# Kernel optimization log

Hardware: AMD Instinct MI355X
Metric: run time of the kernel (lower is better)

The kernel has to match this reference:

```python
import jax, jax.numpy as jnp
import numpy as np
from jax import lax

B, T, IN, H = 128, 1024, 130, 512


def setup_inputs() -> dict:
    key = jax.random.key(0)
    ks = jax.random.split(key, 6)
    inputs = jax.random.normal(ks[0], (B, T, IN), dtype=jnp.float32)
    # valid lengths in [1, T] (forward indexes outputs[len-1])
    inputs_len = jax.random.randint(ks[1], (B,), 1, T + 1)
    h0 = jnp.zeros((B, H), dtype=jnp.float32)
    c0 = jnp.zeros((B, H), dtype=jnp.float32)
    s = 1.0 / np.sqrt(H)
    W_ih = jax.random.uniform(ks[2], (4 * H, IN - 2), jnp.float32, -s, s)
    W_hh = jax.random.uniform(ks[3], (4 * H, H), jnp.float32, -s, s)
    b_ih = jax.random.uniform(ks[4], (4 * H,), jnp.float32, -s, s)
    b_hh = jax.random.uniform(ks[5], (4 * H,), jnp.float32, -s, s)
    return {"inputs": inputs, "inputs_len": inputs_len, "h0": h0, "c0": c0,
            "W_ih": W_ih, "W_hh": W_hh, "b_ih": b_ih, "b_hh": b_hh}


def _lstm_encode(inputs, h0, c0, W_ih, W_hh, b_ih, b_hh):
    # drop last 2 features (coordinates), as in stard_LSTM branch
    x = inputs[..., :-2]                                   # [B, T, IN-2]
    # precompute input projections for all timesteps (same math as per-step)
    xproj = jnp.einsum('bti,gi->tbg', x, W_ih) + b_ih + b_hh  # [T, B, 4H]

    def step(carry, xw):
        h, c = carry
        gates = xw + h @ W_hh.T                            # [B, 4H]
        i, f, g, o = jnp.split(gates, 4, axis=-1)
        i = jax.nn.sigmoid(i)
        f = jax.nn.sigmoid(f)
        g = jnp.tanh(g)
        o = jax.nn.sigmoid(o)
        c2 = f * c + i * g
        h2 = o * jnp.tanh(c2)
        return (h2, c2), h2

    _, hs = lax.scan(step, (h0, c0), xproj)                # hs: [T, B, H]
    return hs


def reference(inputs, inputs_len, h0, c0, W_ih, W_hh, b_ih, b_hh):
    hs = _lstm_encode(inputs, h0, c0, W_ih, W_hh, b_ih, b_hh)
    # gather hidden state at last valid timestep per sequence
    b_idx = jnp.arange(inputs.shape[0])
    return hs[inputs_len - 1, b_idx]                       # [B, H]
```

## Files before the change

### kernel.cpp

```cpp
#include <hip/hip_runtime.h>
#include <hip/hip_bf16.h>
#include <cstdint>
#include <cstddef>

#define T_STEPS 1024
#define BATCH   128
#define INF     128
#define HID     512
#define NBLK    256
#define NTHR    256
#define PK      648

typedef _Float16 f16x8 __attribute__((ext_vector_type(8)));
typedef float    f32x4 __attribute__((ext_vector_type(4)));

static __device__ __forceinline__ unsigned short f16b(float v) {
  _Float16 h = (_Float16)v;
  unsigned short u;
  __builtin_memcpy(&u, &h, 2);
  return u;
}
static __device__ __forceinline__ float fsigmoid(float x) {
  return 1.f / (1.f + __expf(-x));
}
static __device__ __forceinline__ float ftanh(float x) {
  return 1.f - 2.f / (__expf(2.f * x) + 1.f);
}


__global__ __launch_bounds__(256) void k_prep_x(const float* __restrict__ in,
                                                unsigned short* __restrict__ xp)
{
  int t = blockIdx.x >> 3, bg = blockIdx.x & 7;
  int tid = threadIdx.x;
  size_t base = (size_t)blockIdx.x * 2048;
  #pragma unroll
  for (int rep = 0; rep < 8; ++rep) {
    int idx = rep * 256 + tid;
    int c = idx >> 7, k = idx & 127;
    float v = in[((size_t)(bg * 16 + c) * T_STEPS + t) * 130 + k];
    xp[base + c * 128 + k] = f16b(v);
  }
}

__global__ __launch_bounds__(64) void k_prep_w(const float* __restrict__ Wih,
                                               const float* __restrict__ Whh,
                                               unsigned short* __restrict__ wf)
{
  int blk = blockIdx.x;
  int s = blk % 20; int r = blk / 20;
  int u4 = r & 3; int ug = r >> 2;
  int l = threadIdx.x;
  int m = l & 15;
  int Grow = (m & 3) * HID + ug * 16 + u4 * 4 + (m >> 2);
  int kb = s * 32 + (l >> 4) * 8;
  unsigned short o[8];
  #pragma unroll
  for (int j = 0; j < 8; ++j) {
    float v = (kb + j < INF) ? Wih[(size_t)Grow * INF + kb + j]
                             : Whh[(size_t)Grow * HID + (kb + j - INF)];
    o[j] = f16b(v);
  }
  unsigned short* d = wf + ((size_t)blk * 64 + l) * 8;
  #pragma unroll
  for (int j = 0; j < 8; ++j) d[j] = o[j];
}

__global__ __launch_bounds__(256) void k_prep_h(const float* __restrict__ h0,
                                                unsigned long long* __restrict__ hp0,
                                                unsigned long long* __restrict__ hp1)
{
  int idx = blockIdx.x * 256 + threadIdx.x;
  int bg = idx >> 12;
  int r = idx & 4095;
  int c = r >> 8, u2 = r & 255;
  float v0 = h0[(size_t)(bg * 16 + c) * HID + 2 * u2];
  float v1 = h0[(size_t)(bg * 16 + c) * HID + 2 * u2 + 1];
  hp0[idx] = (unsigned long long)((unsigned)f16b(v0) | ((unsigned)f16b(v1) << 16));
  hp1[idx] = 0ull;
}

__global__ __launch_bounds__(NTHR, 1) void k_persist(
    const unsigned short* __restrict__ xp,
    const unsigned short* __restrict__ wf,
    const float* __restrict__ bih, const float* __restrict__ bhh,
    unsigned long long* __restrict__ hp0,
    unsigned long long* __restrict__ hp1,
    const float* __restrict__ c0,
    const int* __restrict__ len,
    float* __restrict__ out)
{
  __shared__ short zpl[2][16][PK];

  const int blk = blockIdx.x;
  const int ug = blk & 31, bg = blk >> 5;
  const int tid = threadIdx.x;
  const int w = tid >> 6, l = tid & 63;
  const int cB = l & 15, gch = l >> 4;

  const uint4* wfq = (const uint4*)wf;
  const int fb = (ug * 4 + w) * 20;
#define LDW(s_) (*reinterpret_cast<const f16x8*>(&wfq[(size_t)(fb + (s_)) * 64 + l]))
  f16x8 A0 = LDW(0),  A1 = LDW(1),  A2 = LDW(2),  A3 = LDW(3),  A4 = LDW(4);
  f16x8 A5 = LDW(5),  A6 = LDW(6),  A7 = LDW(7),  A8 = LDW(8),  A9 = LDW(9);
  f16x8 A10 = LDW(10), A11 = LDW(11), A12 = LDW(12), A13 = LDW(13), A14 = LDW(14);
  f16x8 A15 = LDW(15), A16 = LDW(16), A17 = LDW(17), A18 = LDW(18), A19 = LDW(19);
#undef LDW
  asm volatile("" : "+v"(A0), "+v"(A1), "+v"(A2), "+v"(A3), "+v"(A4),
                    "+v"(A5), "+v"(A6), "+v"(A7), "+v"(A8), "+v"(A9),
                    "+v"(A10), "+v"(A11), "+v"(A12), "+v"(A13), "+v"(A14),
                    "+v"(A15), "+v"(A16), "+v"(A17), "+v"(A18), "+v"(A19));

  const int cb = l & 15;
  const int uloc = l >> 4;
  const int hu = ug * 16 + w * 4 + uloc;
  const int gb = bg * 16 + cb;
  float c_reg = c0[(size_t)gb * HID + hu];
  const int mylen = len[gb];
  float bsq[4];
  #pragma unroll
  for (int g = 0; g < 4; ++g) bsq[g] = bih[g * HID + hu] + bhh[g * HID + hu];

  const int hc = tid >> 4, hs = tid & 15;

  for (int t = 0; t < T_STEPS; ++t) {
    const unsigned long long* hq = ((t & 1) ? hp1 : hp0) + (size_t)bg * 4096;
    unsigned long long*       hd = ((t & 1) ? hp0 : hp1) + (size_t)bg * 4096;
    short (*zb)[PK] = zpl[t & 1];

    uint4 xv = ((const uint4*)(xp + (size_t)(t * 8 + bg) * 2048))[tid];

    unsigned long long hch[16];
    #pragma unroll
    for (int j = 0; j < 16; ++j)
      hch[j] = __hip_atomic_load(hq + hc * 256 + j * 16 + hs,
                                 __ATOMIC_RELAXED, __HIP_MEMORY_SCOPE_AGENT);

    *(uint4*)((char*)&zb[tid >> 4][0] + (tid & 15) * 16) = xv;

    for (;;) {
      int bad = 0;
      #pragma unroll
      for (int j = 0; j < 16; ++j)
        if ((unsigned)(hch[j] >> 32) != (unsigned)t) bad = 1;
      if (!__any(bad)) break;
      __builtin_amdgcn_s_sleep(1);
      #pragma unroll
      for (int j = 0; j < 16; ++j)
        if ((unsigned)(hch[j] >> 32) != (unsigned)t)
          hch[j] = __hip_atomic_load(hq + hc * 256 + j * 16 + hs,
                                     __ATOMIC_RELAXED, __HIP_MEMORY_SCOPE_AGENT);
    }

    {
      unsigned* zr = (unsigned*)&zb[hc][128];
      #pragma unroll
      for (int j = 0; j < 16; ++j)
        zr[j * 16 + hs] = (unsigned)hch[j];
    }
    __syncthreads();

    f32x4 aE = {0, 0, 0, 0}, aO = {0, 0, 0, 0};
    const short* zr = &zb[cB][0];
#define KS(s_, AF, ACC) \
  { f16x8 B = *(const f16x8*)(zr + (s_) * 32 + gch * 8); \
    ACC = __builtin_amdgcn_mfma_f32_16x16x32_f16(AF, B, ACC, 0, 0, 0); }
    KS(0, A0, aE)  KS(1, A1, aO)  KS(2, A2, aE)  KS(3, A3, aO)
    KS(4, A4, aE)  KS(5, A5, aO)  KS(6, A6, aE)  KS(7, A7, aO)
    KS(8, A8, aE)  KS(9, A9, aO)  KS(10, A10, aE) KS(11, A11, aO)
    KS(12, A12, aE) KS(13, A13, aO) KS(14, A14, aE) KS(15, A15, aO)
    KS(16, A16, aE) KS(17, A17, aO) KS(18, A18, aE) KS(19, A19, aO)
#undef KS

    float s0 = aE[0] + aO[0] + bsq[0];
    float s1 = aE[1] + aO[1] + bsq[1];
    float s2 = aE[2] + aO[2] + bsq[2];
    float s3 = aE[3] + aO[3] + bsq[3];
    float iv = fsigmoid(s0);
    float fv = fsigmoid(s1);
    float gv = ftanh(s2);
    float ov = fsigmoid(s3);
    c_reg = fv * c_reg + iv * gv;
    float h2 = ov * ftanh(c_reg);

    unsigned hb = f16b(h2);
    unsigned other = __shfl_xor(hb, 16);
    if ((uloc & 1) == 0) {
      unsigned long long word = ((unsigned long long)(unsigned)(t + 1) << 32)
                              | (unsigned long long)(hb | (other << 16));
      __hip_atomic_store(hd + cb * 256 + (ug * 8 + w * 2 + (uloc >> 1)), word,
                         __ATOMIC_RELAXED, __HIP_MEMORY_SCOPE_AGENT);
    }
    if (t == mylen - 1) out[(size_t)gb * HID + hu] = h2;
  }
}

extern "C" void kernel_launch(void* const* d_in, const int* in_sizes, int n_in,
                              void* d_out, int out_size, void* d_ws, size_t ws_size,
                              hipStream_t stream)
{
  const float* inputs = (const float*)d_in[0];
  const int*   len    = (const int*)  d_in[1];
  const float* h0     = (const float*)d_in[2];
  const float* c0     = (const float*)d_in[3];
  const float* Wih    = (const float*)d_in[4];
  const float* Whh    = (const float*)d_in[5];
  const float* bih    = (const float*)d_in[6];
  const float* bhh    = (const float*)d_in[7];
  float* out = (float*)d_out;

  char* p = (char*)d_ws;
  unsigned short* xp = (unsigned short*)p; p += (size_t)T_STEPS * 8 * 2048 * 2;
  unsigned short* wf = (unsigned short*)p; p += (size_t)2560 * 64 * 8 * 2;
  unsigned long long* hp0 = (unsigned long long*)p; p += (size_t)8 * 4096 * 8;
  unsigned long long* hp1 = (unsigned long long*)p; p += (size_t)8 * 4096 * 8;

  k_prep_x<<<T_STEPS * 8, 256, 0, stream>>>(inputs, xp);
  k_prep_w<<<2560, 64, 0, stream>>>(Wih, Whh, wf);
  k_prep_h<<<128, 256, 0, stream>>>(h0, hp0, hp1);

  void* args[] = {(void*)&xp, (void*)&wf, (void*)&bih, (void*)&bhh,
                  (void*)&hp0, (void*)&hp1, (void*)&c0, (void*)&len,
                  (void*)&out};
  (void)hipLaunchCooperativeKernel((void*)k_persist, dim3(NBLK), dim3(NTHR),
                                   args, 0, stream);
}
```

Before: 3.452 ms.

## Interleave two batch groups per block to overlap h polling with compute

Each persistent block now handles two batch groups (A and B) with one set of register-resident weights, and the grid is halved to 128 blocks. The loop alternates between groups: while one group's MFMA and gate math run, the block issues and polls the other group's hidden-state loads, so cross-block synchronization latency is hidden behind useful work. In exchange, each block does twice the compute serially per step, with fewer blocks spread over the CUs.

```diff
diff --git a/kernel.cpp b/kernel.cpp
--- a/kernel.cpp
+++ b/kernel.cpp
@@ -7,7 +7,7 @@
 #define BATCH   128
 #define INF     128
 #define HID     512
-#define NBLK    256
+#define NBLK    128
 #define NTHR    256
 #define PK      648
 
@@ -90,10 +90,12 @@
     const int* __restrict__ len,
     float* __restrict__ out)
 {
-  __shared__ short zpl[2][16][PK];
+  __shared__ short zplA[16][PK];
+  __shared__ short zplB[16][PK];
 
   const int blk = blockIdx.x;
-  const int ug = blk & 31, bg = blk >> 5;
+  const int ug = blk & 31, pr = blk >> 5;
+  const int bgA = pr * 2, bgB = pr * 2 + 1;
   const int tid = threadIdx.x;
   const int w = tid >> 6, l = tid & 63;
   const int cB = l & 15, gch = l >> 4;
@@ -114,85 +116,129 @@
   const int cb = l & 15;
   const int uloc = l >> 4;
   const int hu = ug * 16 + w * 4 + uloc;
-  const int gb = bg * 16 + cb;
-  float c_reg = c0[(size_t)gb * HID + hu];
-  const int mylen = len[gb];
+  const int gbA = bgA * 16 + cb, gbB = bgB * 16 + cb;
+  float cA  = c0[(size_t)gbA * HID + hu];
+  float cB_ = c0[(size_t)gbB * HID + hu];
+  const int lenA = len[gbA], lenB = len[gbB];
   float bsq[4];
   #pragma unroll
   for (int g = 0; g < 4; ++g) bsq[g] = bih[g * HID + hu] + bhh[g * HID + hu];
 
   const int hc = tid >> 4, hs = tid & 15;
 
+#define HISSUE(HQ, HCH)                                                        \
+  _Pragma("unroll")                                                            \
+  for (int j = 0; j < 16; ++j)                                                 \
+    (HCH)[j] = __hip_atomic_load((HQ) + hc * 256 + j * 16 + hs,                \
+                                 __ATOMIC_RELAXED, __HIP_MEMORY_SCOPE_AGENT);
+
+#define HCHECK(HQ, HCH, TT)                                                    \
+  for (;;) {                                                                   \
+    int bad = 0;                                                               \
+    _Pragma("unroll")                                                          \
+    for (int j = 0; j < 16; ++j)                                               \
+      if ((unsigned)((HCH)[j] >> 32) != (unsigned)(TT)) bad = 1;               \
+    if (!__any(bad)) break;                                                    \
+    __builtin_amdgcn_s_sleep(1);                                               \
+    _Pragma("unroll")                                                          \
+    for (int j = 0; j < 16; ++j)                                               \
+      if ((unsigned)((HCH)[j] >> 32) != (unsigned)(TT))                        \
+        (HCH)[j] = __hip_atomic_load((HQ) + hc * 256 + j * 16 + hs,            \
+                                     __ATOMIC_RELAXED, __HIP_MEMORY_SCOPE_AGENT); \
+  }
+
+#define HSTAGE(ZB, HCH, XV)                                                    \
+  *(uint4*)((char*)&(ZB)[tid >> 4][0] + (tid & 15) * 16) = (XV);               \
+  {                                                                            \
+    unsigned* zr_ = (unsigned*)&(ZB)[hc][128];                                 \
+    _Pragma("unroll")                                                          \
+    for (int j = 0; j < 16; ++j) zr_[j * 16 + hs] = (unsigned)(HCH)[j];        \
+  }
+
+#define KS(ZR, s_, AF, ACC)                                                    \
+  { f16x8 B = *(const f16x8*)((ZR) + (s_) * 32 + gch * 8);                     \
+    ACC = __builtin_amdgcn_mfma_f32_16x16x32_f16(AF, B, ACC, 0, 0, 0); }
+
+#define COMPUTE(ZB, CREG, HD, GB, MYLEN)                                       \
+  {                                                                            \
+    f32x4 aE = {0, 0, 0, 0}, aO = {0, 0, 0, 0};                                \
+    const short* zr_ = &(ZB)[cB][0];                                           \
+    KS(zr_, 0, A0, aE)  KS(zr_, 1, A1, aO)  KS(zr_, 2, A2, aE)                 \
+    KS(zr_, 3, A3, aO)  KS(zr_, 4, A4, aE)  KS(zr_, 5, A5, aO)                 \
+    KS(zr_, 6, A6, aE)  KS(zr_, 7, A7, aO)  KS(zr_, 8, A8, aE)                 \
+    KS(zr_, 9, A9, aO)  KS(zr_, 10, A10, aE) KS(zr_, 11, A11, aO)              \
+    KS(zr_, 12, A12, aE) KS(zr_, 13, A13, aO) KS(zr_, 14, A14, aE)             \
+    KS(zr_, 15, A15, aO) KS(zr_, 16, A16, aE) KS(zr_, 17, A17, aO)             \
+    KS(zr_, 18, A18, aE) KS(zr_, 19, A19, aO)                                  \
+    float s0 = aE[0] + aO[0] + bsq[0];                                         \
+    float s1 = aE[1] + aO[1] + bsq[1];                                         \
+    float s2 = aE[2] + aO[2] + bsq[2];                                         \
+    float s3 = aE[3] + aO[3] + bsq[3];                                         \
+    float iv = fsigmoid(s0), fv = fsigmoid(s1);                                \
+    float gv = ftanh(s2),    ov = fsigmoid(s3);                                \
+    (CREG) = fv * (CREG) + iv * gv;                                            \
+    float h2 = ov * ftanh(CREG);                                               \
+    unsigned hb = f16b(h2);                                                    \
+    unsigned other = __shfl_xor(hb, 16);                                       \
+    if ((uloc & 1) == 0) {                                                     \
+      unsigned long long word =                                                \
+          ((unsigned long long)(unsigned)(t + 1) << 32)                        \
+        | (unsigned long long)(hb | (other << 16));                            \
+      __hip_atomic_store((HD) + cb * 256 + (ug * 8 + w * 2 + (uloc >> 1)),     \
+                         word, __ATOMIC_RELAXED, __HIP_MEMORY_SCOPE_AGENT);    \
+    }                                                                          \
+    if (t == (MYLEN) - 1) out[(size_t)(GB) * HID + hu] = h2;                   \
+  }
+
+  {
+    const int t = 0;  (void)t;
+    uint4 xv = ((const uint4*)(xp + (size_t)(0 * 8 + bgA) * 2048))[tid];
+    const unsigned long long* hq = hp0 + (size_t)bgA * 4096;
+    unsigned long long hch[16];
+    HISSUE(hq, hch)
+    HCHECK(hq, hch, 0)
+    HSTAGE(zplA, hch, xv)
+    __syncthreads();
+  }
+
   for (int t = 0; t < T_STEPS; ++t) {
-    const unsigned long long* hq = ((t & 1) ? hp1 : hp0) + (size_t)bg * 4096;
-    unsigned long long*       hd = ((t & 1) ? hp0 : hp1) + (size_t)bg * 4096;
-    short (*zb)[PK] = zpl[t & 1];
-
-    uint4 xv = ((const uint4*)(xp + (size_t)(t * 8 + bg) * 2048))[tid];
-
-    unsigned long long hch[16];
-    #pragma unroll
-    for (int j = 0; j < 16; ++j)
-      hch[j] = __hip_atomic_load(hq + hc * 256 + j * 16 + hs,
-                                 __ATOMIC_RELAXED, __HIP_MEMORY_SCOPE_AGENT);
-
-    *(uint4*)((char*)&zb[tid >> 4][0] + (tid & 15) * 16) = xv;
-
-    for (;;) {
-      int bad = 0;
-      #pragma unroll
-      for (int j = 0; j < 16; ++j)
-        if ((unsigned)(hch[j] >> 32) != (unsigned)t) bad = 1;
-      if (!__any(bad)) break;
-      __builtin_amdgcn_s_sleep(1);
-      #pragma unroll
-      for (int j = 0; j < 16; ++j)
-        if ((unsigned)(hch[j] >> 32) != (unsigned)t)
-          hch[j] = __hip_atomic_load(hq + hc * 256 + j * 16 + hs,
-                                     __ATOMIC_RELAXED, __HIP_MEMORY_SCOPE_AGENT);
+    const int pn = (t + 1) & 1, pc_ = t & 1;
+    unsigned long long* hdA = (pn ? hp1 : hp0) + (size_t)bgA * 4096;
+    unsigned long long* hdB = (pn ? hp1 : hp0) + (size_t)bgB * 4096;
+    const unsigned long long* hqB = (pc_ ? hp1 : hp0) + (size_t)bgB * 4096;
+
+    unsigned long long hchB[16];
+    uint4 xvB = ((const uint4*)(xp + (size_t)(t * 8 + bgB) * 2048))[tid];
+    HISSUE(hqB, hchB)
+    __builtin_amdgcn_sched_barrier(0);
+
+    COMPUTE(zplA, cA, hdA, gbA, lenA)
+
+    HCHECK(hqB, hchB, t)
+    HSTAGE(zplB, hchB, xvB)
+    __syncthreads();
+
+    if (t + 1 < T_STEPS) {
+      const unsigned long long* hqA = (pn ? hp1 : hp0) + (size_t)bgA * 4096;
+      unsigned long long hchA[16];
+      uint4 xvA = ((const uint4*)(xp + (size_t)((t + 1) * 8 + bgA) * 2048))[tid];
+      HISSUE(hqA, hchA)
+      __builtin_amdgcn_sched_barrier(0);
+
+      COMPUTE(zplB, cB_, hdB, gbB, lenB)
+
+      HCHECK(hqA, hchA, t + 1)
+      HSTAGE(zplA, hchA, xvA)
+      __syncthreads();
+    } else {
+      COMPUTE(zplB, cB_, hdB, gbB, lenB)
     }
-
-    {
-      unsigned* zr = (unsigned*)&zb[hc][128];
-      #pragma unroll
-      for (int j = 0; j < 16; ++j)
-        zr[j * 16 + hs] = (unsigned)hch[j];
-    }
-    __syncthreads();
-
-    f32x4 aE = {0, 0, 0, 0}, aO = {0, 0, 0, 0};
-    const short* zr = &zb[cB][0];
-#define KS(s_, AF, ACC) \
-  { f16x8 B = *(const f16x8*)(zr + (s_) * 32 + gch * 8); \
-    ACC = __builtin_amdgcn_mfma_f32_16x16x32_f16(AF, B, ACC, 0, 0, 0); }
-    KS(0, A0, aE)  KS(1, A1, aO)  KS(2, A2, aE)  KS(3, A3, aO)
-    KS(4, A4, aE)  KS(5, A5, aO)  KS(6, A6, aE)  KS(7, A7, aO)
-    KS(8, A8, aE)  KS(9, A9, aO)  KS(10, A10, aE) KS(11, A11, aO)
-    KS(12, A12, aE) KS(13, A13, aO) KS(14, A14, aE) KS(15, A15, aO)
-    KS(16, A16, aE) KS(17, A17, aO) KS(18, A18, aE) KS(19, A19, aO)
+  }
+#undef COMPUTE
 #undef KS
-
-    float s0 = aE[0] + aO[0] + bsq[0];
-    float s1 = aE[1] + aO[1] + bsq[1];
-    float s2 = aE[2] + aO[2] + bsq[2];
-    float s3 = aE[3] + aO[3] + bsq[3];
-    float iv = fsigmoid(s0);
-    float fv = fsigmoid(s1);
-    float gv = ftanh(s2);
-    float ov = fsigmoid(s3);
-    c_reg = fv * c_reg + iv * gv;
-    float h2 = ov * ftanh(c_reg);
-
-    unsigned hb = f16b(h2);
-    unsigned other = __shfl_xor(hb, 16);
-    if ((uloc & 1) == 0) {
-      unsigned long long word = ((unsigned long long)(unsigned)(t + 1) << 32)
-                              | (unsigned long long)(hb | (other << 16));
-      __hip_atomic_store(hd + cb * 256 + (ug * 8 + w * 2 + (uloc >> 1)), word,
-                         __ATOMIC_RELAXED, __HIP_MEMORY_SCOPE_AGENT);
-    }
-    if (t == mylen - 1) out[(size_t)gb * HID + hu] = h2;
-  }
+#undef HSTAGE
+#undef HCHECK
+#undef HISSUE
 }
 
 extern "C" void kernel_launch(void* const* d_in, const int* in_sizes, int n_in,
```

Result: slower. 4.046 ms (+17.2%).
